# Performance work log

Measured on AMD Instinct MI355X. Metric: run time of the kernel, lower is better.

The kernel has to match this reference:

```python
import jax, jax.numpy as jnp
import numpy as np

N = 50000
E = 600000
C = 128      # in_channels
H = 2 * C    # GENConv MLP hidden
OUT = 128    # encoder out_channels
EPS_GEN = 1e-7
EPS_BN = 1e-5


def batchnorm(h, g, b):
    m = h.mean(axis=0)
    v = ((h - m) ** 2).mean(axis=0)  # biased var, torch train-mode norm
    return (h - m) * jax.lax.rsqrt(v + EPS_BN) * g + b


def setup_inputs() -> dict:
    key = jax.random.key(0)
    ks = jax.random.split(key, 12)
    s = 0.05
    return {
        "x": jax.random.normal(ks[0], (N, C), dtype=jnp.float32),
        "edge_index": jax.random.randint(ks[1], (2, E), 0, N, dtype=jnp.int64),
        # outer DeepGCNLayer BatchNorm (affine)
        "bn_g": jnp.ones((C,), jnp.float32),
        "bn_b": jnp.zeros((C,), jnp.float32),
        # GENConv MLP: Linear(C,2C) -> BN -> ReLU -> Linear(2C,2C) -> BN -> ReLU -> Linear(2C,C)
        "W1": jax.random.normal(ks[2], (C, H), jnp.float32) * s,
        "b1": jnp.zeros((H,), jnp.float32),
        "g1": jnp.ones((H,), jnp.float32),
        "be1": jnp.zeros((H,), jnp.float32),
        "W2": jax.random.normal(ks[3], (H, H), jnp.float32) * s,
        "b2": jnp.zeros((H,), jnp.float32),
        "g2": jnp.ones((H,), jnp.float32),
        "be2": jnp.zeros((H,), jnp.float32),
        "W3": jax.random.normal(ks[4], (H, C), jnp.float32) * s,
        "b3": jnp.zeros((C,), jnp.float32),
        # encoder Linear(C, OUT)
        "We": jax.random.normal(ks[5], (C, OUT), jnp.float32) * s,
        "be": jnp.zeros((OUT,), jnp.float32),
    }


def gen_conv(h, src, dst, W1, b1, g1, be1, W2, b2, g2, be2, W3, b3):
    # message: relu(x_j) + eps  (no edge_attr)
    msg = jax.nn.relu(h[src]) + EPS_GEN                     # [E, C]
    # softmax aggregation over edges grouped by dst (t=1.0)
    mx = jax.ops.segment_max(msg, dst, num_segments=N)      # [N, C]
    mx = jnp.where(jnp.isfinite(mx), mx, 0.0)
    ex = jnp.exp(msg - mx[dst])                             # [E, C]
    den = jax.ops.segment_sum(ex, dst, num_segments=N)      # [N, C]
    alpha = ex / (den[dst] + 1e-16)
    agg = jax.ops.segment_sum(msg * alpha, dst, num_segments=N)  # [N, C]
    out = agg + h                                           # root added before MLP
    h1 = jax.nn.relu(batchnorm(out @ W1 + b1, g1, be1))
    h2 = jax.nn.relu(batchnorm(h1 @ W2 + b2, g2, be2))
    return h2 @ W3 + b3


def reference(x, edge_index, bn_g, bn_b, W1, b1, g1, be1, W2, b2, g2, be2,
              W3, b3, We, be):
    src = edge_index[0]
    dst = edge_index[1]
    # DeepGCNLayer 'res+': h = conv(dropout(act(norm(x)))); out = x + h
    # (dropout p=0.05 treated as identity / eval mode for determinism)
    h = jax.nn.relu(batchnorm(x, bn_g, bn_b))
    h = gen_conv(h, src, dst, W1, b1, g1, be1, W2, b2, g2, be2, W3, b3)
    out = x + h
    return out @ We + be
```

## Files before the change

### kernel.cpp

```cpp
#include <hip/hip_runtime.h>
#include <cstddef>
#include <cstdint>

#define NN 50000
#define NE 600000
#define CC 128
#define HD 256
#define NC (NN * CC)
#define EPS_GEN 1e-7f
#define EPS_BN  1e-5f

typedef __attribute__((ext_vector_type(8))) short short8;
typedef __attribute__((ext_vector_type(4))) float f32x4;

__device__ inline ushort f2bf(float f) {
    uint u = __float_as_uint(f);
    return (ushort)((u + 0x7FFFu + ((u >> 16) & 1u)) >> 16);
}

__global__ __launch_bounds__(256)
void stats_kernel(const float* __restrict__ A, int M, int Ncols,
                  float* __restrict__ sum, float* __restrict__ sumsq)
{
    int col = threadIdx.x % Ncols;
    int rowInBlock = threadIdx.x / Ncols;
    int rowsPerBlock = blockDim.x / Ncols;
    int step = rowsPerBlock * gridDim.x;
    float s = 0.f, q = 0.f;
    for (int r = blockIdx.x * rowsPerBlock + rowInBlock; r < M; r += step) {
        float v = A[(size_t)r * Ncols + col];
        s += v;
        q = fmaf(v, v, q);
    }
    atomicAdd(&sum[col], s);
    atomicAdd(&sumsq[col], q);
}

__global__ void finalize_bn(const float* __restrict__ sum,
                            const float* __restrict__ sumsq,
                            const float* __restrict__ g,
                            const float* __restrict__ b,
                            float* __restrict__ scale,
                            float* __restrict__ shift,
                            int M, int Ncols)
{
    int c = blockIdx.x * blockDim.x + threadIdx.x;
    if (c >= Ncols) return;
    float inv_m = 1.0f / (float)M;
    float mean = sum[c] * inv_m;
    float var  = sumsq[c] * inv_m - mean * mean;
    float v = var + EPS_BN;
    float rs = rsqrtf(v);
    rs = rs * (1.5f - 0.5f * v * rs * rs);
    float sc = g[c] * rs;
    scale[c] = sc;
    shift[c] = b[c] - mean * sc;
}

template <int NCOL>
__global__ __launch_bounds__(256)
void bnrelu_kernel(const float* __restrict__ src,
                   const float* __restrict__ scale,
                   const float* __restrict__ shift,
                   float* __restrict__ dst, int total4)
{
    int tid = blockIdx.x * blockDim.x + threadIdx.x;
    if (tid >= total4) return;
    int c4 = tid & (NCOL / 4 - 1);
    float4 sc = ((const float4*)scale)[c4];
    float4 sh = ((const float4*)shift)[c4];
    float4 v  = ((const float4*)src)[tid];
    float4 o;
    o.x = fmaxf(fmaf(v.x, sc.x, sh.x), 0.f);
    o.y = fmaxf(fmaf(v.y, sc.y, sh.y), 0.f);
    o.z = fmaxf(fmaf(v.z, sc.z, sh.z), 0.f);
    o.w = fmaxf(fmaf(v.w, sc.w, sh.w), 0.f);
    ((float4*)dst)[tid] = o;
}

__global__ __launch_bounds__(256)
void hist_kernel(const int* __restrict__ dst, int* __restrict__ deg)
{
    int e = blockIdx.x * blockDim.x + threadIdx.x;
    if (e < NE) atomicAdd(&deg[dst[e]], 1);
}

__global__ __launch_bounds__(1024)
void scan_kernel(const int* __restrict__ deg, int* __restrict__ rowptr, int n)
{
    __shared__ int wsum[16];
    __shared__ int woff[16];
    int lane = threadIdx.x & 63, wid = threadIdx.x >> 6;
    if (threadIdx.x == 0) rowptr[0] = 0;
    int carry = 0;
    for (int base = 0; base < n; base += 1024) {
        int i = base + threadIdx.x;
        int v = (i < n) ? deg[i] : 0;
        int s = v;
        #pragma unroll
        for (int off = 1; off < 64; off <<= 1) {
            int t = __shfl_up(s, off, 64);
            if (lane >= off) s += t;
        }
        if (lane == 63) wsum[wid] = s;
        __syncthreads();
        if (wid == 0) {
            int ws = (lane < 16) ? wsum[lane] : 0;
            #pragma unroll
            for (int off = 1; off < 16; off <<= 1) {
                int t = __shfl_up(ws, off, 64);
                if (lane >= off) ws += t;
            }
            if (lane < 16) woff[lane] = ws;
        }
        __syncthreads();
        int blockoff = (wid > 0) ? woff[wid - 1] : 0;
        if (i < n) rowptr[i + 1] = carry + s + blockoff;
        carry += woff[15];
        __syncthreads();
    }
}

__global__ __launch_bounds__(256)
void scatter_kernel(const int* __restrict__ src, const int* __restrict__ dst,
                    const int* __restrict__ rowptr, int* __restrict__ cursor,
                    int* __restrict__ col)
{
    int e = blockIdx.x * blockDim.x + threadIdx.x;
    if (e >= NE) return;
    int d = dst[e];
    int pos = atomicAdd(&cursor[d], 1);
    col[rowptr[d] + pos] = src[e];
}

__global__ __launch_bounds__(128)
void csr_agg_kernel(const int* __restrict__ rowptr, const int* __restrict__ col,
                    const float* __restrict__ h, float* __restrict__ a0)
{
    int node = blockIdx.x;
    int c = threadIdx.x;
    int beg = rowptr[node], end = rowptr[node + 1];
    float den = 0.f, num = 0.f;
    for (int j = beg; j < end; j++) {
        int s = col[j];
        float msg = h[(size_t)s * CC + c] + EPS_GEN;
        float ex = __expf(msg);
        den += ex;
        num = fmaf(msg, ex, num);
    }
    float hv = h[(size_t)node * CC + c];
    a0[(size_t)node * CC + c] = num / (den + 1e-16f) + hv;
}

template <bool RESID>
__global__ __launch_bounds__(256)
void gemm_bf16(const float* __restrict__ A, const float* __restrict__ B,
               const float* __restrict__ bias, const float* __restrict__ resid,
               float* __restrict__ C, int M, int K, int Nn)
{
    __shared__ __align__(16) ushort As[64 * 32];
    __shared__ __align__(16) ushort Bs[64 * 32];
    const int bm = blockIdx.y * 64, bn = blockIdx.x * 64;
    const int t = threadIdx.x;
    const int w = t >> 6, lane = t & 63;
    const int wr = w >> 1, wc = w & 1;
    const int l16 = lane & 15, g = lane >> 4;

    f32x4 acc[2][2];
    #pragma unroll
    for (int i = 0; i < 2; i++)
        #pragma unroll
        for (int j = 0; j < 2; j++) {
            f32x4 z = {0.f, 0.f, 0.f, 0.f};
            acc[i][j] = z;
        }

    for (int k0 = 0; k0 < K; k0 += 32) {
        #pragma unroll
        for (int p = 0; p < 2; p++) {
            int rl = (t >> 3) + 32 * p;
            int kc = (t & 7) * 4;
            int row = bm + rl;
            float4 v = {0.f, 0.f, 0.f, 0.f};
            if (row < M) v = *(const float4*)&A[(size_t)row * K + k0 + kc];
            uint lo = (uint)f2bf(v.x) | ((uint)f2bf(v.y) << 16);
            uint hi = (uint)f2bf(v.z) | ((uint)f2bf(v.w) << 16);
            int el = (rl * 32 + kc) ^ ((rl & 7) << 3);
            *(uint2*)&As[el] = make_uint2(lo, hi);
        }
        {
            int n = t & 63, kk0 = t >> 6;
            #pragma unroll
            for (int i = 0; i < 8; i++) {
                int kk = kk0 + 4 * i;
                ushort bv = f2bf(B[(size_t)(k0 + kk) * Nn + bn + n]);
                int el = (n * 32 + kk) ^ ((n & 7) << 3);
                Bs[el] = bv;
            }
        }
        __syncthreads();

        short8 af[2], bfr[2];
        #pragma unroll
        for (int fm = 0; fm < 2; fm++) {
            int m = 32 * wr + 16 * fm + l16;
            int el = (m * 32 + 8 * g) ^ ((m & 7) << 3);
            af[fm] = *(const short8*)&As[el];
        }
        #pragma unroll
        for (int fn = 0; fn < 2; fn++) {
            int n = 32 * wc + 16 * fn + l16;
            int el = (n * 32 + 8 * g) ^ ((n & 7) << 3);
            bfr[fn] = *(const short8*)&Bs[el];
        }
        #pragma unroll
        for (int fm = 0; fm < 2; fm++)
            #pragma unroll
            for (int fn = 0; fn < 2; fn++)
                acc[fm][fn] = __builtin_amdgcn_mfma_f32_16x16x32_bf16(
                    af[fm], bfr[fn], acc[fm][fn], 0, 0, 0);
        __syncthreads();
    }

    #pragma unroll
    for (int fn = 0; fn < 2; fn++) {
        int colg = bn + 32 * wc + 16 * fn + l16;
        float bv = bias[colg];
        #pragma unroll
        for (int fm = 0; fm < 2; fm++) {
            #pragma unroll
            for (int r = 0; r < 4; r++) {
                int row = bm + 32 * wr + 16 * fm + 4 * g + r;
                if (row < M) {
                    float val = acc[fm][fn][r] + bv;
                    if (RESID) val += resid[(size_t)row * Nn + colg];
                    C[(size_t)row * Nn + colg] = val;
                }
            }
        }
    }
}

extern "C" void kernel_launch(void* const* d_in, const int* in_sizes, int n_in,
                              void* d_out, int out_size, void* d_ws, size_t ws_size,
                              hipStream_t stream)
{
    const float* x    = (const float*)d_in[0];
    const int*   ei   = (const int*)d_in[1];
    const int*   srcE = ei;
    const int*   dstE = ei + NE;
    const float* bn_g = (const float*)d_in[2];
    const float* bn_b = (const float*)d_in[3];
    const float* W1   = (const float*)d_in[4];
    const float* b1   = (const float*)d_in[5];
    const float* g1   = (const float*)d_in[6];
    const float* be1  = (const float*)d_in[7];
    const float* W2   = (const float*)d_in[8];
    const float* b2   = (const float*)d_in[9];
    const float* g2   = (const float*)d_in[10];
    const float* be2  = (const float*)d_in[11];
    const float* W3   = (const float*)d_in[12];
    const float* b3   = (const float*)d_in[13];
    const float* We   = (const float*)d_in[14];
    const float* beb  = (const float*)d_in[15];
    float* out = (float*)d_out;

    float* ws = (float*)d_ws;
    float* sum0   = ws + 0;    float* sq0    = ws + 128;
    float* scale0 = ws + 256;  float* shift0 = ws + 384;
    float* sum1   = ws + 512;  float* sq1    = ws + 768;
    float* scale1 = ws + 1024; float* shift1 = ws + 1280;
    float* sum2   = ws + 1536; float* sq2    = ws + 1792;
    float* scale2 = ws + 2048; float* shift2 = ws + 2304;
    float* buf0 = ws + 4096;
    float* buf1 = buf0 + NC;
    float* buf2 = buf1 + NC;
    float* buf3 = buf2 + NC;
    float* h  = buf0;
    float* a0 = buf1;
    float* t1 = buf2;
    float* t2 = buf0;
    float* y  = buf2;
    (void)buf3;

    int* ipool  = (int*)buf2;
    int* deg    = ipool;
    int* cursor = ipool + 50176;
    int* rowptr = ipool + 100352;
    int* col    = ipool + 151040;

    hipMemsetAsync(ws, 0, 4096 * sizeof(float), stream);
    hipMemsetAsync(ipool, 0, 100352 * sizeof(int), stream);

    stats_kernel<<<128, 256, 0, stream>>>(x, NN, CC, sum0, sq0);
    finalize_bn<<<1, 128, 0, stream>>>(sum0, sq0, bn_g, bn_b, scale0, shift0, NN, CC);
    bnrelu_kernel<CC><<<(NC / 4 + 255) / 256, 256, 0, stream>>>(x, scale0, shift0, h, NC / 4);

    hist_kernel<<<(NE + 255) / 256, 256, 0, stream>>>(dstE, deg);
    scan_kernel<<<1, 1024, 0, stream>>>(deg, rowptr, NN);
    scatter_kernel<<<(NE + 255) / 256, 256, 0, stream>>>(srcE, dstE, rowptr, cursor, col);
    csr_agg_kernel<<<NN, 128, 0, stream>>>(rowptr, col, h, a0);

    const int MB = (NN + 63) / 64;
    const int NC2 = NN * HD;
    gemm_bf16<false><<<dim3(HD / 64, MB), 256, 0, stream>>>(
        a0, W1, b1, nullptr, t1, NN, CC, HD);
    stats_kernel<<<128, 256, 0, stream>>>(t1, NN, HD, sum1, sq1);
    finalize_bn<<<1, 256, 0, stream>>>(sum1, sq1, g1, be1, scale1, shift1, NN, HD);
    bnrelu_kernel<HD><<<(NC2 / 4 + 255) / 256, 256, 0, stream>>>(t1, scale1, shift1, t1, NC2 / 4);

    gemm_bf16<false><<<dim3(HD / 64, MB), 256, 0, stream>>>(
        t1, W2, b2, nullptr, t2, NN, HD, HD);
    stats_kernel<<<128, 256, 0, stream>>>(t2, NN, HD, sum2, sq2);
    finalize_bn<<<1, 256, 0, stream>>>(sum2, sq2, g2, be2, scale2, shift2, NN, HD);
    bnrelu_kernel<HD><<<(NC2 / 4 + 255) / 256, 256, 0, stream>>>(t2, scale2, shift2, t2, NC2 / 4);

    gemm_bf16<true><<<dim3(CC / 64, MB), 256, 0, stream>>>(
        t2, W3, b3, x, y, NN, HD, CC);
    gemm_bf16<false><<<dim3(CC / 64, MB), 256, 0, stream>>>(
        y, We, beb, nullptr, out, NN, CC, CC);
}
```

Baseline: 684.2 us.

## Fuse BN+ReLU into GEMM A-load and vectorize column statistics kernel

Removes the two standalone bnrelu passes over the 50000x256 hidden activations by applying scale/shift/ReLU while loading A tiles in the following GEMM. Replaces the scalar stats kernel with a float4-vectorized version that reduces partial sums in shared memory before issuing atomics, and launches it with more blocks. This cuts full read+write passes over large intermediates, at the cost of extra per-tile loads of scale/shift and extra ALU in the GEMM load path.

```diff
diff --git a/kernel.cpp b/kernel.cpp
--- a/kernel.cpp
+++ b/kernel.cpp
@@ -18,22 +18,52 @@
     return (ushort)((u + 0x7FFFu + ((u >> 16) & 1u)) >> 16);
 }
 
-__global__ __launch_bounds__(256)
-void stats_kernel(const float* __restrict__ A, int M, int Ncols,
-                  float* __restrict__ sum, float* __restrict__ sumsq)
-{
-    int col = threadIdx.x % Ncols;
-    int rowInBlock = threadIdx.x / Ncols;
-    int rowsPerBlock = blockDim.x / Ncols;
-    int step = rowsPerBlock * gridDim.x;
-    float s = 0.f, q = 0.f;
-    for (int r = blockIdx.x * rowsPerBlock + rowInBlock; r < M; r += step) {
-        float v = A[(size_t)r * Ncols + col];
-        s += v;
-        q = fmaf(v, v, q);
-    }
-    atomicAdd(&sum[col], s);
-    atomicAdd(&sumsq[col], q);
+template <int NCOL>
+__global__ __launch_bounds__(256)
+void stats4_kernel(const float* __restrict__ A, int M,
+                   float* __restrict__ sum, float* __restrict__ sumsq)
+{
+    constexpr int G = NCOL / 4;
+    constexpr int R = 256 / G;
+    __shared__ float4 s_lds[256];
+    __shared__ float4 q_lds[256];
+    const int c = threadIdx.x % G;
+    const int r = threadIdx.x / G;
+    float4 s = {0.f, 0.f, 0.f, 0.f}, q = {0.f, 0.f, 0.f, 0.f};
+    const int step = R * gridDim.x;
+    for (int row = blockIdx.x * R + r; row < M; row += step) {
+        float4 v = ((const float4*)(A + (size_t)row * NCOL))[c];
+        s.x += v.x; s.y += v.y; s.z += v.z; s.w += v.w;
+        q.x = fmaf(v.x, v.x, q.x);
+        q.y = fmaf(v.y, v.y, q.y);
+        q.z = fmaf(v.z, v.z, q.z);
+        q.w = fmaf(v.w, v.w, q.w);
+    }
+    s_lds[threadIdx.x] = s;
+    q_lds[threadIdx.x] = q;
+    __syncthreads();
+    #pragma unroll
+    for (int st = R / 2; st > 0; st >>= 1) {
+        if (r < st) {
+            float4 s2 = s_lds[threadIdx.x + st * G];
+            float4 q2 = q_lds[threadIdx.x + st * G];
+            s.x += s2.x; s.y += s2.y; s.z += s2.z; s.w += s2.w;
+            q.x += q2.x; q.y += q2.y; q.z += q2.z; q.w += q2.w;
+            s_lds[threadIdx.x] = s;
+            q_lds[threadIdx.x] = q;
+        }
+        __syncthreads();
+    }
+    if (r == 0) {
+        atomicAdd(&sum[c * 4 + 0], s.x);
+        atomicAdd(&sum[c * 4 + 1], s.y);
+        atomicAdd(&sum[c * 4 + 2], s.z);
+        atomicAdd(&sum[c * 4 + 3], s.w);
+        atomicAdd(&sumsq[c * 4 + 0], q.x);
+        atomicAdd(&sumsq[c * 4 + 1], q.y);
+        atomicAdd(&sumsq[c * 4 + 2], q.z);
+        atomicAdd(&sumsq[c * 4 + 3], q.w);
+    }
 }
 
 __global__ void finalize_bn(const float* __restrict__ sum,
@@ -152,10 +182,12 @@
     a0[(size_t)node * CC + c] = num / (den + 1e-16f) + hv;
 }
 
-template <bool RESID>
+template <bool TRANSA, bool RESID>
 __global__ __launch_bounds__(256)
 void gemm_bf16(const float* __restrict__ A, const float* __restrict__ B,
-               const float* __restrict__ bias, const float* __restrict__ resid,
+               const float* __restrict__ bias,
+               const float* __restrict__ asc, const float* __restrict__ ash,
+               const float* __restrict__ resid,
                float* __restrict__ C, int M, int K, int Nn)
 {
     __shared__ __align__(16) ushort As[64 * 32];
@@ -183,6 +215,14 @@
             int row = bm + rl;
             float4 v = {0.f, 0.f, 0.f, 0.f};
             if (row < M) v = *(const float4*)&A[(size_t)row * K + k0 + kc];
+            if (TRANSA) {
+                float4 sc = *(const float4*)&asc[k0 + kc];
+                float4 sh = *(const float4*)&ash[k0 + kc];
+                v.x = fmaxf(fmaf(v.x, sc.x, sh.x), 0.f);
+                v.y = fmaxf(fmaf(v.y, sc.y, sh.y), 0.f);
+                v.z = fmaxf(fmaf(v.z, sc.z, sh.z), 0.f);
+                v.w = fmaxf(fmaf(v.w, sc.w, sh.w), 0.f);
+            }
             uint lo = (uint)f2bf(v.x) | ((uint)f2bf(v.y) << 16);
             uint hi = (uint)f2bf(v.z) | ((uint)f2bf(v.w) << 16);
             int el = (rl * 32 + kc) ^ ((rl & 7) << 3);
@@ -292,7 +332,7 @@
     hipMemsetAsync(ws, 0, 4096 * sizeof(float), stream);
     hipMemsetAsync(ipool, 0, 100352 * sizeof(int), stream);
 
-    stats_kernel<<<128, 256, 0, stream>>>(x, NN, CC, sum0, sq0);
+    stats4_kernel<CC><<<512, 256, 0, stream>>>(x, NN, sum0, sq0);
     finalize_bn<<<1, 128, 0, stream>>>(sum0, sq0, bn_g, bn_b, scale0, shift0, NN, CC);
     bnrelu_kernel<CC><<<(NC / 4 + 255) / 256, 256, 0, stream>>>(x, scale0, shift0, h, NC / 4);
 
@@ -302,21 +342,18 @@
     csr_agg_kernel<<<NN, 128, 0, stream>>>(rowptr, col, h, a0);
 
     const int MB = (NN + 63) / 64;
-    const int NC2 = NN * HD;
-    gemm_bf16<false><<<dim3(HD / 64, MB), 256, 0, stream>>>(
-        a0, W1, b1, nullptr, t1, NN, CC, HD);
-    stats_kernel<<<128, 256, 0, stream>>>(t1, NN, HD, sum1, sq1);
+    gemm_bf16<false, false><<<dim3(HD / 64, MB), 256, 0, stream>>>(
+        a0, W1, b1, nullptr, nullptr, nullptr, t1, NN, CC, HD);
+    stats4_kernel<HD><<<512, 256, 0, stream>>>(t1, NN, sum1, sq1);
     finalize_bn<<<1, 256, 0, stream>>>(sum1, sq1, g1, be1, scale1, shift1, NN, HD);
-    bnrelu_kernel<HD><<<(NC2 / 4 + 255) / 256, 256, 0, stream>>>(t1, scale1, shift1, t1, NC2 / 4);
-
-    gemm_bf16<false><<<dim3(HD / 64, MB), 256, 0, stream>>>(
-        t1, W2, b2, nullptr, t2, NN, HD, HD);
-    stats_kernel<<<128, 256, 0, stream>>>(t2, NN, HD, sum2, sq2);
+
+    gemm_bf16<true, false><<<dim3(HD / 64, MB), 256, 0, stream>>>(
+        t1, W2, b2, scale1, shift1, nullptr, t2, NN, HD, HD);
+    stats4_kernel<HD><<<512, 256, 0, stream>>>(t2, NN, sum2, sq2);
     finalize_bn<<<1, 256, 0, stream>>>(sum2, sq2, g2, be2, scale2, shift2, NN, HD);
-    bnrelu_kernel<HD><<<(NC2 / 4 + 255) / 256, 256, 0, stream>>>(t2, scale2, shift2, t2, NC2 / 4);
-
-    gemm_bf16<true><<<dim3(CC / 64, MB), 256, 0, stream>>>(
-        t2, W3, b3, x, y, NN, HD, CC);
-    gemm_bf16<false><<<dim3(CC / 64, MB), 256, 0, stream>>>(
-        y, We, beb, nullptr, out, NN, CC, CC);
-}
+
+    gemm_bf16<true, true><<<dim3(CC / 64, MB), 256, 0, stream>>>(
+        t2, W3, b3, scale2, shift2, x, y, NN, HD, CC);
+    gemm_bf16<false, false><<<dim3(CC / 64, MB), 256, 0, stream>>>(
+        y, We, beb, nullptr, nullptr, nullptr, out, NN, CC, CC);
+}
```

New measurement: 604.8 us. 11.6% less time.
